# Kernel optimization log

Measured on AMD Instinct MI355X. Metric: run time of the kernel, lower is better.

The kernel has to match this reference:

```python
import jax, jax.numpy as jnp
import numpy as np

D_MODEL = 128
N_STATE = 64
SPATIAL = (128, 128)
BATCH = 4


def _ssm_kernel(log_A_real, A_imag, log_dt, Bk, Ck, L):
    # log_A_real: (D,N), A_imag: (N,), log_dt: (D,), Bk/Ck: (D,N) complex
    dt = jnp.exp(log_dt)[:, None]                      # (D,1)
    A = -jnp.exp(log_A_real) + 1j * A_imag[None, :]    # (D,N) complex
    t = jnp.arange(L, dtype=jnp.float32)               # (L,)
    # A_bar**t computed in log domain: exp(t * A * dt)  -> (D,L,N)
    A_pow = jnp.exp((A * dt)[:, None, :] * t[None, :, None])
    # K = sum_n C*B*A_bar^t  (note: original uses B, not B_bar)
    return jnp.einsum('dn,dln->dl', Ck * Bk, A_pow)    # (D,L) complex


def setup_inputs() -> dict:
    key = jax.random.key(0)
    ks = jax.random.split(key, 12)
    sh_u = (BATCH, D_MODEL) + SPATIAL
    return {
        'u_re': jax.random.normal(ks[0], sh_u, jnp.float32),
        'u_im': jax.random.normal(ks[1], sh_u, jnp.float32),
        'log_A_real': jnp.log(0.5 * jnp.ones((2, D_MODEL, N_STATE), jnp.float32)),
        'A_imag': jnp.tile((jnp.pi * jnp.arange(N_STATE, dtype=jnp.float32) / N_STATE)[None], (2, 1)),
        'Bp_re': jax.random.normal(ks[2], (2, D_MODEL, N_STATE), jnp.float32),
        'Bp_im': jax.random.normal(ks[3], (2, D_MODEL, N_STATE), jnp.float32),
        'Cp_re': jax.random.normal(ks[4], (2, D_MODEL, N_STATE), jnp.float32),
        'Cp_im': jax.random.normal(ks[5], (2, D_MODEL, N_STATE), jnp.float32),
        'log_dt': jax.random.uniform(ks[6], (2, D_MODEL), jnp.float32) * (np.log(0.1) - np.log(0.001)) + np.log(0.001),
        'W_re': jax.random.normal(ks[7], (D_MODEL, D_MODEL), jnp.float32) / np.sqrt(D_MODEL),
        'W_im': jax.random.normal(ks[8], (D_MODEL, D_MODEL), jnp.float32) / np.sqrt(D_MODEL),
    }


def reference(u_re, u_im, log_A_real, A_imag, Bp_re, Bp_im, Cp_re, Cp_im, log_dt, W_re, W_im):
    u = u_re + 1j * u_im                               # (B,C,L1,L2) complex
    L1, L2 = u.shape[2], u.shape[3]
    B0 = Bp_re + 1j * Bp_im
    C0 = Cp_re + 1j * Cp_im
    k0 = _ssm_kernel(log_A_real[0], A_imag[0], log_dt[0], B0[0], C0[0], L1)  # (C,L1)
    k1 = _ssm_kernel(log_A_real[1], A_imag[1], log_dt[1], B0[1], C0[1], L2)  # (C,L2)
    k_global = k0[:, :, None] * k1[:, None, :]          # (C,L1,L2)
    pad = (2 * L1, 2 * L2)
    axes = (-2, -1)
    u_f = jnp.fft.fftn(u, s=pad, axes=axes)
    k_f = jnp.fft.fftn(k_global, s=pad, axes=axes)
    y = jnp.fft.ifftn(u_f * k_f, s=pad, axes=axes)[:, :, :L1, :L2]  # (B,C,L1,L2)
    # (B,L1,L2,C) -> complex linear (bias=False, torch: x @ W^T) -> back to (B,C,L1,L2)
    y = jnp.transpose(y, (0, 2, 3, 1))
    W = W_re + 1j * W_im
    y = jnp.einsum('bxyc,dc->bxyd', y, W)               # activation=identity, dropout=eval identity
    return jnp.transpose(y, (0, 3, 1, 2))
```

## Files before the change

### kernel.cpp

```cpp
#include <hip/hip_runtime.h>

#define B_ 4
#define C_ 128
#define L_ 128
#define N_ 64
#define KPAD 7

__global__ __launch_bounds__(256) void compute_k_kernel(
    const float* __restrict__ logA, const float* __restrict__ Aim,
    const float* __restrict__ Bre, const float* __restrict__ Bim,
    const float* __restrict__ Cre, const float* __restrict__ Cim,
    const float* __restrict__ logdt, float* __restrict__ kbuf)
{
    int idx = blockIdx.x * 256 + threadIdx.x;
    int axis = idx >> 14;
    int c = (idx >> 7) & 127;
    int t = idx & 127;
    float dt = expf(logdt[axis * C_ + c]);
    float tf = (float)t;
    const float* lA = logA + (axis * C_ + c) * N_;
    const float* br = Bre + (axis * C_ + c) * N_;
    const float* bi = Bim + (axis * C_ + c) * N_;
    const float* cr = Cre + (axis * C_ + c) * N_;
    const float* ci = Cim + (axis * C_ + c) * N_;
    const float* ai = Aim + axis * N_;
    float kr = 0.f, ki = 0.f;
    for (int n = 0; n < N_; ++n) {
        float zre = -expf(lA[n]) * dt;
        float zim = ai[n] * dt;
        float mag = expf(zre * tf);
        float s, co;
        sincosf(zim * tf, &s, &co);
        float wr = mag * co, wi = mag * s;
        float cbr = cr[n] * br[n] - ci[n] * bi[n];
        float cbi = cr[n] * bi[n] + ci[n] * br[n];
        kr += cbr * wr - cbi * wi;
        ki += cbr * wi + cbi * wr;
    }
    kbuf[axis * 32768 + c * L_ + t] = kr;
    kbuf[axis * 32768 + 16384 + c * L_ + t] = ki;
}

__global__ __launch_bounds__(512) void conv2d_kernel(
    const float* __restrict__ u_re, const float* __restrict__ u_im,
    const float* __restrict__ kbuf, float* __restrict__ z_re, float* __restrict__ z_im)
{
    __shared__ __align__(16) float br[128][128];
    __shared__ __align__(16) float bi[128][128];
    __shared__ float kx0r[136], kx0i[136], kx1r[136], kx1i[136];
    int bc = blockIdx.x;
    int c = bc & 127;
    int tid = threadIdx.x;
    if (tid < 136) {
        int t = tid - KPAD;
        bool v = (t >= 0 && t < 128);
        kx0r[tid] = v ? kbuf[c * 128 + t] : 0.f;
        kx0i[tid] = v ? kbuf[16384 + c * 128 + t] : 0.f;
        kx1r[tid] = v ? kbuf[32768 + c * 128 + t] : 0.f;
        kx1i[tid] = v ? kbuf[49152 + c * 128 + t] : 0.f;
    }
    size_t gbase = (size_t)bc * 16384;
    {
        int r = tid >> 2, q = tid & 3;
        const float4* gr = (const float4*)(u_re + gbase + r * 128 + q * 32);
        const float4* gi = (const float4*)(u_im + gbase + r * 128 + q * 32);
        float4* lr = (float4*)&br[r][q * 32];
        float4* li = (float4*)&bi[r][q * 32];
#pragma unroll
        for (int m = 0; m < 8; ++m) { lr[m] = gr[m]; li[m] = gi[m]; }
    }
    __syncthreads();

    int xq = tid >> 4;
    int yq = tid & 15;
    int x0 = xq << 2;
    int yb = yq << 2;
    float ar[4][8], ai_[4][8];
#pragma unroll
    for (int k = 0; k < 4; ++k)
#pragma unroll
        for (int m = 0; m < 8; ++m) { ar[k][m] = 0.f; ai_[k][m] = 0.f; }
    for (int a = 0; a < 128; ++a) {
        float4 u0 = *(const float4*)&br[a][yb];
        float4 u1 = *(const float4*)&br[a][64 + yb];
        float4 v0 = *(const float4*)&bi[a][yb];
        float4 v1 = *(const float4*)&bi[a][64 + yb];
        float ur[8] = {u0.x, u0.y, u0.z, u0.w, u1.x, u1.y, u1.z, u1.w};
        float ui[8] = {v0.x, v0.y, v0.z, v0.w, v1.x, v1.y, v1.z, v1.w};
        int j = x0 - a + KPAD; j = j < 0 ? 0 : j;
#pragma unroll
        for (int k = 0; k < 4; ++k) {
            float kr = kx0r[j + k], ki = kx0i[j + k];
#pragma unroll
            for (int m = 0; m < 8; ++m) {
                ar[k][m] += kr * ur[m] - ki * ui[m];
                ai_[k][m] += kr * ui[m] + ki * ur[m];
            }
        }
    }
    __syncthreads();
#pragma unroll
    for (int m = 0; m < 8; ++m) {
        int y = (m < 4) ? (yb + m) : (64 + yb + m - 4);
        *(float4*)&br[y][x0] = make_float4(ar[0][m], ar[1][m], ar[2][m], ar[3][m]);
        *(float4*)&bi[y][x0] = make_float4(ai_[0][m], ai_[1][m], ai_[2][m], ai_[3][m]);
    }
    __syncthreads();

    int xq2 = tid & 15;
    int yq2 = tid >> 4;
    int xb = xq2 << 2;
    int y0 = yq2 << 2;
    float cr[4][8], ci_[4][8];
#pragma unroll
    for (int k = 0; k < 4; ++k)
#pragma unroll
        for (int m = 0; m < 8; ++m) { cr[k][m] = 0.f; ci_[k][m] = 0.f; }
    for (int j = 0; j < 128; ++j) {
        float4 z0 = *(const float4*)&br[j][xb];
        float4 z1v = *(const float4*)&br[j][64 + xb];
        float4 w0 = *(const float4*)&bi[j][xb];
        float4 w1 = *(const float4*)&bi[j][64 + xb];
        float zr[8] = {z0.x, z0.y, z0.z, z0.w, z1v.x, z1v.y, z1v.z, z1v.w};
        float zi[8] = {w0.x, w0.y, w0.z, w0.w, w1.x, w1.y, w1.z, w1.w};
        int j2 = y0 - j + KPAD; j2 = j2 < 0 ? 0 : j2;
#pragma unroll
        for (int k = 0; k < 4; ++k) {
            float kr = kx1r[j2 + k], ki = kx1i[j2 + k];
#pragma unroll
            for (int m = 0; m < 8; ++m) {
                cr[k][m] += kr * zr[m] - ki * zi[m];
                ci_[k][m] += kr * zi[m] + ki * zr[m];
            }
        }
    }
    __syncthreads();
#pragma unroll
    for (int m = 0; m < 8; ++m) {
        int x = (m < 4) ? (xb + m) : (64 + xb + m - 4);
        *(float4*)&br[x][y0] = make_float4(cr[0][m], cr[1][m], cr[2][m], cr[3][m]);
        *(float4*)&bi[x][y0] = make_float4(ci_[0][m], ci_[1][m], ci_[2][m], ci_[3][m]);
    }
    __syncthreads();
    {
        int r = tid >> 2, q = tid & 3;
        float4* gr = (float4*)(z_re + gbase + r * 128 + q * 32);
        float4* gi = (float4*)(z_im + gbase + r * 128 + q * 32);
#pragma unroll
        for (int m = 0; m < 8; ++m) {
            gr[m] = *(float4*)&br[r][q * 32 + 4 * m];
            gi[m] = *(float4*)&bi[r][q * 32 + 4 * m];
        }
    }
}

__global__ __launch_bounds__(256) void mix_kernel(
    float* __restrict__ z_re, const float* __restrict__ z_im,
    const float* __restrict__ Wre, const float* __restrict__ Wim)
{
    __shared__ __align__(16) float zr_s[32][128];
    __shared__ __align__(16) float zi_s[32][128];
    __shared__ __align__(16) float wr_s[32][132];
    __shared__ __align__(16) float wi_s[32][132];
    int bid = blockIdx.x;
    int b = bid >> 7;
    int s0 = (bid & 127) << 7;
    int tid = threadIdx.x;
    int sq = tid & 15;
    int dq = tid >> 4;
    float acc[8][8];
#pragma unroll
    for (int di = 0; di < 8; ++di)
#pragma unroll
        for (int si = 0; si < 8; ++si) acc[di][si] = 0.f;

    for (int c0 = 0; c0 < 128; c0 += 32) {
        __syncthreads();
#pragma unroll
        for (int it = 0; it < 4; ++it) {
            int idx4 = it * 256 + tid;
            int cc = idx4 >> 5, sR = (idx4 & 31) << 2;
            *(float4*)&zr_s[cc][sR] =
                *(const float4*)&z_re[(size_t)(b * 128 + c0 + cc) * 16384 + s0 + sR];
            *(float4*)&zi_s[cc][sR] =
                *(const float4*)&z_im[(size_t)(b * 128 + c0 + cc) * 16384 + s0 + sR];
        }
#pragma unroll
        for (int it = 0; it < 4; ++it) {
            int idx4 = it * 256 + tid;
            int d = idx4 >> 3, ccR = (idx4 & 7) << 2;
            float4 wr = *(const float4*)&Wre[d * 128 + c0 + ccR];
            float4 wi = *(const float4*)&Wim[d * 128 + c0 + ccR];
            wr_s[ccR + 0][d] = wr.x; wr_s[ccR + 1][d] = wr.y;
            wr_s[ccR + 2][d] = wr.z; wr_s[ccR + 3][d] = wr.w;
            wi_s[ccR + 0][d] = wi.x; wi_s[ccR + 1][d] = wi.y;
            wi_s[ccR + 2][d] = wi.z; wi_s[ccR + 3][d] = wi.w;
        }
        __syncthreads();
        for (int cc = 0; cc < 32; ++cc) {
            float4 a0 = *(const float4*)&wr_s[cc][4 * dq];
            float4 a1 = *(const float4*)&wr_s[cc][64 + 4 * dq];
            float4 b0 = *(const float4*)&wi_s[cc][4 * dq];
            float4 b1 = *(const float4*)&wi_s[cc][64 + 4 * dq];
            float4 c0v = *(const float4*)&zr_s[cc][4 * sq];
            float4 c1v = *(const float4*)&zr_s[cc][64 + 4 * sq];
            float4 d0v = *(const float4*)&zi_s[cc][4 * sq];
            float4 d1v = *(const float4*)&zi_s[cc][64 + 4 * sq];
            float wr[8] = {a0.x, a0.y, a0.z, a0.w, a1.x, a1.y, a1.z, a1.w};
            float wi[8] = {b0.x, b0.y, b0.z, b0.w, b1.x, b1.y, b1.z, b1.w};
            float zr[8] = {c0v.x, c0v.y, c0v.z, c0v.w, c1v.x, c1v.y, c1v.z, c1v.w};
            float zi[8] = {d0v.x, d0v.y, d0v.z, d0v.w, d1v.x, d1v.y, d1v.z, d1v.w};
#pragma unroll
            for (int di = 0; di < 8; ++di)
#pragma unroll
                for (int si = 0; si < 8; ++si)
                    acc[di][si] += wr[di] * zr[si] - wi[di] * zi[si];
        }
    }
    __syncthreads();
#pragma unroll
    for (int di = 0; di < 8; ++di) {
        int d = (di < 4) ? (4 * dq + di) : (64 + 4 * dq + di - 4);
        float* o = z_re + (size_t)(b * 128 + d) * 16384 + s0;
        *(float4*)&o[4 * sq] = make_float4(acc[di][0], acc[di][1], acc[di][2], acc[di][3]);
        *(float4*)&o[64 + 4 * sq] = make_float4(acc[di][4], acc[di][5], acc[di][6], acc[di][7]);
    }
}

extern "C" void kernel_launch(void* const* d_in, const int* in_sizes, int n_in,
                              void* d_out, int out_size, void* d_ws, size_t ws_size,
                              hipStream_t stream) {
    const float* u_re  = (const float*)d_in[0];
    const float* u_im  = (const float*)d_in[1];
    const float* logA  = (const float*)d_in[2];
    const float* Aim   = (const float*)d_in[3];
    const float* Bre   = (const float*)d_in[4];
    const float* Bim   = (const float*)d_in[5];
    const float* Cre   = (const float*)d_in[6];
    const float* Cim   = (const float*)d_in[7];
    const float* logdt = (const float*)d_in[8];
    const float* Wre   = (const float*)d_in[9];
    const float* Wim   = (const float*)d_in[10];
    float* kbuf = (float*)d_ws;
    float* z_im = (float*)d_ws + 65536;
    float* z_re = (float*)d_out;

    hipLaunchKernelGGL(compute_k_kernel, dim3(128), dim3(256), 0, stream,
                       logA, Aim, Bre, Bim, Cre, Cim, logdt, kbuf);
    hipLaunchKernelGGL(conv2d_kernel, dim3(B_ * C_), dim3(512), 0, stream,
                       u_re, u_im, kbuf, z_re, z_im);
    hipLaunchKernelGGL(mix_kernel, dim3(B_ * 128), dim3(256), 0, stream,
                       z_re, z_im, Wre, Wim);
}
```

Baseline: 470.5 us.

## Split 2D causal conv into per-axis kernels with triangular skipping and swizzled LDS

Replaces the single-block 2D convolution with two separable kernels, one for x and one for y. Each kernel handles half of a (batch, channel) plane per block. The inner loop only runs up to the causal bound, so the zero upper triangle of the Toeplitz product is skipped, and the halves are assigned in reverse order to even out the work. LDS rows use an XOR swizzle to avoid bank conflicts, and LDS use per block is halved, which allows more resident blocks. The cost is an extra global round trip of the intermediate between the two passes. The channel-mix tile depth is also reduced to 16.

```diff
diff --git a/kernel.cpp b/kernel.cpp
--- a/kernel.cpp
+++ b/kernel.cpp
@@ -4,7 +4,18 @@
 #define C_ 128
 #define L_ 128
 #define N_ 64
-#define KPAD 7
+
+__device__ __forceinline__ float fget(const float4& v, int e) {
+    switch (e) { case 0: return v.x; case 1: return v.y; case 2: return v.z; default: return v.w; }
+}
+
+__device__ __forceinline__ void cfma(float4& ar, float4& ai, float kr, float ki,
+                                     const float4& vr, const float4& vi) {
+    ar.x += kr * vr.x - ki * vi.x; ai.x += kr * vi.x + ki * vr.x;
+    ar.y += kr * vr.y - ki * vi.y; ai.y += kr * vi.y + ki * vr.y;
+    ar.z += kr * vr.z - ki * vi.z; ai.z += kr * vi.z + ki * vr.z;
+    ar.w += kr * vr.w - ki * vi.w; ai.w += kr * vi.w + ki * vr.w;
+}
 
 __global__ __launch_bounds__(256) void compute_k_kernel(
     const float* __restrict__ logA, const float* __restrict__ Aim,
@@ -41,175 +52,198 @@
     kbuf[axis * 32768 + 16384 + c * L_ + t] = ki;
 }
 
-__global__ __launch_bounds__(512) void conv2d_kernel(
+__global__ __launch_bounds__(512) void conv_x_kernel(
     const float* __restrict__ u_re, const float* __restrict__ u_im,
     const float* __restrict__ kbuf, float* __restrict__ z_re, float* __restrict__ z_im)
 {
-    __shared__ __align__(16) float br[128][128];
-    __shared__ __align__(16) float bi[128][128];
-    __shared__ float kx0r[136], kx0i[136], kx1r[136], kx1i[136];
-    int bc = blockIdx.x;
-    int c = bc & 127;
+    __shared__ float sre[128 * 64];
+    __shared__ float sim[128 * 64];
+    __shared__ float ktr[136], kti[136];
+    int blk = blockIdx.x;
+    int half = blk & 1;
+    int c = (blk >> 1) & 127;
+    int b = blk >> 8;
     int tid = threadIdx.x;
     if (tid < 136) {
-        int t = tid - KPAD;
-        bool v = (t >= 0 && t < 128);
-        kx0r[tid] = v ? kbuf[c * 128 + t] : 0.f;
-        kx0i[tid] = v ? kbuf[16384 + c * 128 + t] : 0.f;
-        kx1r[tid] = v ? kbuf[32768 + c * 128 + t] : 0.f;
-        kx1i[tid] = v ? kbuf[49152 + c * 128 + t] : 0.f;
-    }
-    size_t gbase = (size_t)bc * 16384;
-    {
-        int r = tid >> 2, q = tid & 3;
-        const float4* gr = (const float4*)(u_re + gbase + r * 128 + q * 32);
-        const float4* gi = (const float4*)(u_im + gbase + r * 128 + q * 32);
-        float4* lr = (float4*)&br[r][q * 32];
-        float4* li = (float4*)&bi[r][q * 32];
-#pragma unroll
-        for (int m = 0; m < 8; ++m) { lr[m] = gr[m]; li[m] = gi[m]; }
-    }
-    __syncthreads();
-
-    int xq = tid >> 4;
-    int yq = tid & 15;
-    int x0 = xq << 2;
-    int yb = yq << 2;
-    float ar[4][8], ai_[4][8];
-#pragma unroll
-    for (int k = 0; k < 4; ++k)
-#pragma unroll
-        for (int m = 0; m < 8; ++m) { ar[k][m] = 0.f; ai_[k][m] = 0.f; }
-    for (int a = 0; a < 128; ++a) {
-        float4 u0 = *(const float4*)&br[a][yb];
-        float4 u1 = *(const float4*)&br[a][64 + yb];
-        float4 v0 = *(const float4*)&bi[a][yb];
-        float4 v1 = *(const float4*)&bi[a][64 + yb];
-        float ur[8] = {u0.x, u0.y, u0.z, u0.w, u1.x, u1.y, u1.z, u1.w};
-        float ui[8] = {v0.x, v0.y, v0.z, v0.w, v1.x, v1.y, v1.z, v1.w};
-        int j = x0 - a + KPAD; j = j < 0 ? 0 : j;
+        int t = tid - 7;
+        bool v = (t >= 0) && (t < 128);
+        ktr[tid] = v ? kbuf[c * 128 + t] : 0.f;
+        kti[tid] = v ? kbuf[16384 + c * 128 + t] : 0.f;
+    }
+    size_t base = (size_t)(b * 128 + c) * 16384;
+#pragma unroll
+    for (int it = 0; it < 4; ++it) {
+        int i4 = it * 512 + tid;
+        int r = i4 >> 4, c4 = i4 & 15;
+        float4 vr = *(const float4*)(u_re + base + r * 128 + half * 64 + 4 * c4);
+        float4 vi = *(const float4*)(u_im + base + r * 128 + half * 64 + 4 * c4);
+        int p = r * 64 + 4 * (c4 ^ (r & 15));
+        *(float4*)&sre[p] = vr;
+        *(float4*)&sim[p] = vi;
+    }
+    __syncthreads();
+    int w = tid >> 6;
+    int wb = half ? (7 - w) : w;
+    int lane = tid & 63;
+    int rq = 4 * wb + ((lane >> 4) & 3);
+    int cq = lane & 15;
+    int r0 = 4 * rq;
+    int abound = 16 * wb + 15;
+    float4 accr[4], acci[4];
+#pragma unroll
+    for (int k = 0; k < 4; ++k) {
+        accr[k] = make_float4(0.f, 0.f, 0.f, 0.f);
+        acci[k] = make_float4(0.f, 0.f, 0.f, 0.f);
+    }
+    for (int a = 0; a <= abound; ++a) {
+        int p = a * 64 + 4 * (cq ^ (a & 15));
+        float4 vr = *(const float4*)&sre[p];
+        float4 vi = *(const float4*)&sim[p];
+        int jb = r0 - a + 7;
 #pragma unroll
         for (int k = 0; k < 4; ++k) {
-            float kr = kx0r[j + k], ki = kx0i[j + k];
-#pragma unroll
-            for (int m = 0; m < 8; ++m) {
-                ar[k][m] += kr * ur[m] - ki * ui[m];
-                ai_[k][m] += kr * ui[m] + ki * ur[m];
-            }
-        }
-    }
-    __syncthreads();
-#pragma unroll
-    for (int m = 0; m < 8; ++m) {
-        int y = (m < 4) ? (yb + m) : (64 + yb + m - 4);
-        *(float4*)&br[y][x0] = make_float4(ar[0][m], ar[1][m], ar[2][m], ar[3][m]);
-        *(float4*)&bi[y][x0] = make_float4(ai_[0][m], ai_[1][m], ai_[2][m], ai_[3][m]);
-    }
-    __syncthreads();
-
-    int xq2 = tid & 15;
-    int yq2 = tid >> 4;
-    int xb = xq2 << 2;
-    int y0 = yq2 << 2;
-    float cr[4][8], ci_[4][8];
-#pragma unroll
-    for (int k = 0; k < 4; ++k)
-#pragma unroll
-        for (int m = 0; m < 8; ++m) { cr[k][m] = 0.f; ci_[k][m] = 0.f; }
-    for (int j = 0; j < 128; ++j) {
-        float4 z0 = *(const float4*)&br[j][xb];
-        float4 z1v = *(const float4*)&br[j][64 + xb];
-        float4 w0 = *(const float4*)&bi[j][xb];
-        float4 w1 = *(const float4*)&bi[j][64 + xb];
-        float zr[8] = {z0.x, z0.y, z0.z, z0.w, z1v.x, z1v.y, z1v.z, z1v.w};
-        float zi[8] = {w0.x, w0.y, w0.z, w0.w, w1.x, w1.y, w1.z, w1.w};
-        int j2 = y0 - j + KPAD; j2 = j2 < 0 ? 0 : j2;
+            int j = jb + k; j = j < 0 ? 0 : j;
+            cfma(accr[k], acci[k], ktr[j], kti[j], vr, vi);
+        }
+    }
+#pragma unroll
+    for (int k = 0; k < 4; ++k) {
+        *(float4*)(z_re + base + (size_t)(r0 + k) * 128 + half * 64 + 4 * cq) = accr[k];
+        *(float4*)(z_im + base + (size_t)(r0 + k) * 128 + half * 64 + 4 * cq) = acci[k];
+    }
+}
+
+__global__ __launch_bounds__(512) void conv_y_kernel(
+    float* __restrict__ z_re ,
+    float* __restrict__ z_im ,
+    const float* __restrict__ kbuf)
+{
+    __shared__ float sre[128 * 64];
+    __shared__ float sim[128 * 64];
+    __shared__ float ktr[136], kti[136];
+    int blk = blockIdx.x;
+    int half = blk & 1;
+    int c = (blk >> 1) & 127;
+    int b = blk >> 8;
+    int tid = threadIdx.x;
+    if (tid < 136) {
+        int t = tid - 7;
+        bool v = (t >= 0) && (t < 128);
+        ktr[tid] = v ? kbuf[32768 + c * 128 + t] : 0.f;
+        kti[tid] = v ? kbuf[49152 + c * 128 + t] : 0.f;
+    }
+    size_t base = (size_t)(b * 128 + c) * 16384;
+#pragma unroll
+    for (int it = 0; it < 4; ++it) {
+        int i4 = it * 512 + tid;
+        int xl = i4 >> 5, q = i4 & 31;
+        float4 vr = *(const float4*)(z_re + base + (size_t)(half * 64 + xl) * 128 + 4 * q);
+        float4 vi = *(const float4*)(z_im + base + (size_t)(half * 64 + xl) * 128 + 4 * q);
+        int c4 = xl >> 2, e0 = xl & 3;
+#pragma unroll
+        for (int e = 0; e < 4; ++e) {
+            int y = 4 * q + e;
+            int p = y * 64 + 4 * (c4 ^ (y & 15)) + e0;
+            sre[p] = fget(vr, e);
+            sim[p] = fget(vi, e);
+        }
+    }
+    __syncthreads();
+    int w = tid >> 6;
+    int wb = half ? (7 - w) : w;
+    int lane = tid & 63;
+    int rq = 4 * wb + ((lane >> 4) & 3);
+    int cq = lane & 15;
+    int r0 = 4 * rq;
+    int abound = 16 * wb + 15;
+    float4 accr[4], acci[4];
+#pragma unroll
+    for (int k = 0; k < 4; ++k) {
+        accr[k] = make_float4(0.f, 0.f, 0.f, 0.f);
+        acci[k] = make_float4(0.f, 0.f, 0.f, 0.f);
+    }
+    for (int a = 0; a <= abound; ++a) {
+        int p = a * 64 + 4 * (cq ^ (a & 15));
+        float4 vr = *(const float4*)&sre[p];
+        float4 vi = *(const float4*)&sim[p];
+        int jb = r0 - a + 7;
 #pragma unroll
         for (int k = 0; k < 4; ++k) {
-            float kr = kx1r[j2 + k], ki = kx1i[j2 + k];
-#pragma unroll
-            for (int m = 0; m < 8; ++m) {
-                cr[k][m] += kr * zr[m] - ki * zi[m];
-                ci_[k][m] += kr * zi[m] + ki * zr[m];
-            }
-        }
-    }
-    __syncthreads();
-#pragma unroll
-    for (int m = 0; m < 8; ++m) {
-        int x = (m < 4) ? (xb + m) : (64 + xb + m - 4);
-        *(float4*)&br[x][y0] = make_float4(cr[0][m], cr[1][m], cr[2][m], cr[3][m]);
-        *(float4*)&bi[x][y0] = make_float4(ci_[0][m], ci_[1][m], ci_[2][m], ci_[3][m]);
-    }
-    __syncthreads();
-    {
-        int r = tid >> 2, q = tid & 3;
-        float4* gr = (float4*)(z_re + gbase + r * 128 + q * 32);
-        float4* gi = (float4*)(z_im + gbase + r * 128 + q * 32);
-#pragma unroll
-        for (int m = 0; m < 8; ++m) {
-            gr[m] = *(float4*)&br[r][q * 32 + 4 * m];
-            gi[m] = *(float4*)&bi[r][q * 32 + 4 * m];
-        }
+            int j = jb + k; j = j < 0 ? 0 : j;
+            cfma(accr[k], acci[k], ktr[j], kti[j], vr, vi);
+        }
+    }
+    __syncthreads();
+#pragma unroll
+    for (int e = 0; e < 4; ++e) {
+        int cc = 4 * cq + e;
+        int p = cc * 128 + 4 * (rq ^ (cc >> 2));
+        *(float4*)&sre[p] = make_float4(fget(accr[0], e), fget(accr[1], e), fget(accr[2], e), fget(accr[3], e));
+        *(float4*)&sim[p] = make_float4(fget(acci[0], e), fget(acci[1], e), fget(acci[2], e), fget(acci[3], e));
+    }
+    __syncthreads();
+    int cc = tid >> 3, fq = tid & 7;
+#pragma unroll
+    for (int mm = 0; mm < 4; ++mm) {
+        int o4 = fq + 8 * mm;
+        int p = cc * 128 + 4 * (o4 ^ (cc >> 2));
+        float4 vre = *(float4*)&sre[p];
+        float4 vim = *(float4*)&sim[p];
+        *(float4*)(z_im + base + (size_t)(half * 64 + cc) * 128 + 4 * o4) = vre;
+        *(float4*)(z_re + base + (size_t)(half * 64 + cc) * 128 + 4 * o4) = vim;
     }
 }
 
 __global__ __launch_bounds__(256) void mix_kernel(
-    float* __restrict__ z_re, const float* __restrict__ z_im,
+    float* __restrict__ zre , const float* __restrict__ zim ,
     const float* __restrict__ Wre, const float* __restrict__ Wim)
 {
-    __shared__ __align__(16) float zr_s[32][128];
-    __shared__ __align__(16) float zi_s[32][128];
-    __shared__ __align__(16) float wr_s[32][132];
-    __shared__ __align__(16) float wi_s[32][132];
+    __shared__ float zr_s[16][128];
+    __shared__ float zi_s[16][128];
+    __shared__ float wr_s[16][132];
+    __shared__ float wi_s[16][132];
     int bid = blockIdx.x;
-    int b = bid >> 7;
-    int s0 = (bid & 127) << 7;
+    int b = bid >> 7, x = bid & 127;
     int tid = threadIdx.x;
-    int sq = tid & 15;
-    int dq = tid >> 4;
+    int sq = tid & 15, dq = tid >> 4;
     float acc[8][8];
 #pragma unroll
     for (int di = 0; di < 8; ++di)
 #pragma unroll
         for (int si = 0; si < 8; ++si) acc[di][si] = 0.f;
 
-    for (int c0 = 0; c0 < 128; c0 += 32) {
+    for (int c0 = 0; c0 < 128; c0 += 16) {
         __syncthreads();
 #pragma unroll
-        for (int it = 0; it < 4; ++it) {
-            int idx4 = it * 256 + tid;
-            int cc = idx4 >> 5, sR = (idx4 & 31) << 2;
-            *(float4*)&zr_s[cc][sR] =
-                *(const float4*)&z_re[(size_t)(b * 128 + c0 + cc) * 16384 + s0 + sR];
-            *(float4*)&zi_s[cc][sR] =
-                *(const float4*)&z_im[(size_t)(b * 128 + c0 + cc) * 16384 + s0 + sR];
-        }
-#pragma unroll
-        for (int it = 0; it < 4; ++it) {
-            int idx4 = it * 256 + tid;
-            int d = idx4 >> 3, ccR = (idx4 & 7) << 2;
-            float4 wr = *(const float4*)&Wre[d * 128 + c0 + ccR];
-            float4 wi = *(const float4*)&Wim[d * 128 + c0 + ccR];
-            wr_s[ccR + 0][d] = wr.x; wr_s[ccR + 1][d] = wr.y;
-            wr_s[ccR + 2][d] = wr.z; wr_s[ccR + 3][d] = wr.w;
-            wi_s[ccR + 0][d] = wi.x; wi_s[ccR + 1][d] = wi.y;
-            wi_s[ccR + 2][d] = wi.z; wi_s[ccR + 3][d] = wi.w;
+        for (int it = 0; it < 2; ++it) {
+            int i4 = it * 256 + tid;
+            int cc = i4 >> 5, y4 = i4 & 31;
+            size_t g = (size_t)(b * 128 + c0 + cc) * 16384 + x * 128 + 4 * y4;
+            *(float4*)&zr_s[cc][4 * y4] = *(const float4*)(zre + g);
+            *(float4*)&zi_s[cc][4 * y4] = *(const float4*)(zim + g);
+        }
+#pragma unroll
+        for (int it = 0; it < 8; ++it) {
+            int i = it * 256 + tid;
+            int d = i >> 4, cc = i & 15;
+            wr_s[cc][d] = Wre[d * 128 + c0 + cc];
+            wi_s[cc][d] = Wim[d * 128 + c0 + cc];
         }
         __syncthreads();
-        for (int cc = 0; cc < 32; ++cc) {
-            float4 a0 = *(const float4*)&wr_s[cc][4 * dq];
-            float4 a1 = *(const float4*)&wr_s[cc][64 + 4 * dq];
-            float4 b0 = *(const float4*)&wi_s[cc][4 * dq];
-            float4 b1 = *(const float4*)&wi_s[cc][64 + 4 * dq];
-            float4 c0v = *(const float4*)&zr_s[cc][4 * sq];
-            float4 c1v = *(const float4*)&zr_s[cc][64 + 4 * sq];
-            float4 d0v = *(const float4*)&zi_s[cc][4 * sq];
-            float4 d1v = *(const float4*)&zi_s[cc][64 + 4 * sq];
-            float wr[8] = {a0.x, a0.y, a0.z, a0.w, a1.x, a1.y, a1.z, a1.w};
-            float wi[8] = {b0.x, b0.y, b0.z, b0.w, b1.x, b1.y, b1.z, b1.w};
-            float zr[8] = {c0v.x, c0v.y, c0v.z, c0v.w, c1v.x, c1v.y, c1v.z, c1v.w};
-            float zi[8] = {d0v.x, d0v.y, d0v.z, d0v.w, d1v.x, d1v.y, d1v.z, d1v.w};
+#pragma unroll
+        for (int cc = 0; cc < 16; ++cc) {
+            float4 w0 = *(float4*)&wr_s[cc][4 * dq];
+            float4 w1 = *(float4*)&wr_s[cc][64 + 4 * dq];
+            float4 v0 = *(float4*)&wi_s[cc][4 * dq];
+            float4 v1 = *(float4*)&wi_s[cc][64 + 4 * dq];
+            float4 r0v = *(float4*)&zr_s[cc][4 * sq];
+            float4 r1v = *(float4*)&zr_s[cc][64 + 4 * sq];
+            float4 i0v = *(float4*)&zi_s[cc][4 * sq];
+            float4 i1v = *(float4*)&zi_s[cc][64 + 4 * sq];
+            float wr[8] = {w0.x, w0.y, w0.z, w0.w, w1.x, w1.y, w1.z, w1.w};
+            float wi[8] = {v0.x, v0.y, v0.z, v0.w, v1.x, v1.y, v1.z, v1.w};
+            float zr[8] = {r0v.x, r0v.y, r0v.z, r0v.w, r1v.x, r1v.y, r1v.z, r1v.w};
+            float zi[8] = {i0v.x, i0v.y, i0v.z, i0v.w, i1v.x, i1v.y, i1v.z, i1v.w};
 #pragma unroll
             for (int di = 0; di < 8; ++di)
 #pragma unroll
@@ -217,11 +251,10 @@
                     acc[di][si] += wr[di] * zr[si] - wi[di] * zi[si];
         }
     }
-    __syncthreads();
 #pragma unroll
     for (int di = 0; di < 8; ++di) {
         int d = (di < 4) ? (4 * dq + di) : (64 + 4 * dq + di - 4);
-        float* o = z_re + (size_t)(b * 128 + d) * 16384 + s0;
+        float* o = zre + (size_t)(b * 128 + d) * 16384 + x * 128;
         *(float4*)&o[4 * sq] = make_float4(acc[di][0], acc[di][1], acc[di][2], acc[di][3]);
         *(float4*)&o[64 + 4 * sq] = make_float4(acc[di][4], acc[di][5], acc[di][6], acc[di][7]);
     }
@@ -242,13 +275,15 @@
     const float* Wre   = (const float*)d_in[9];
     const float* Wim   = (const float*)d_in[10];
     float* kbuf = (float*)d_ws;
-    float* z_im = (float*)d_ws + 65536;
-    float* z_re = (float*)d_out;
+    float* wsA  = (float*)d_ws + 65536;
+    float* outp = (float*)d_out;
 
     hipLaunchKernelGGL(compute_k_kernel, dim3(128), dim3(256), 0, stream,
                        logA, Aim, Bre, Bim, Cre, Cim, logdt, kbuf);
-    hipLaunchKernelGGL(conv2d_kernel, dim3(B_ * C_), dim3(512), 0, stream,
-                       u_re, u_im, kbuf, z_re, z_im);
+    hipLaunchKernelGGL(conv_x_kernel, dim3(B_ * C_ * 2), dim3(512), 0, stream,
+                       u_re, u_im, kbuf, wsA, outp);
+    hipLaunchKernelGGL(conv_y_kernel, dim3(B_ * C_ * 2), dim3(512), 0, stream,
+                       wsA, outp, kbuf);
     hipLaunchKernelGGL(mix_kernel, dim3(B_ * 128), dim3(256), 0, stream,
-                       z_re, z_im, Wre, Wim);
-}
+                       outp, wsA, Wre, Wim);
+}
```

New measurement: 513.9 us. +9.2%, slower.
